# Kernel optimization log

Measured on AMD Instinct MI355X. Metric: run time of the kernel, lower is better.

The kernel has to match this reference:

```python
import jax, jax.numpy as jnp
import numpy as np

N = 100000   # nodes
E = 1600000  # edges (avg degree 16)
IN = 24
HID = 128
OUT = 12


def setup_inputs() -> dict:
    key = jax.random.key(0)
    ks = jax.random.split(key, 16)
    s = 0.05
    return {
        "inputs": jax.random.normal(ks[0], (N, IN), jnp.float32),
        "src": jax.random.randint(ks[1], (E,), 0, N),
        "dst": jax.random.randint(ks[2], (E,), 0, N),
        "e_w": jax.random.uniform(ks[3], (E, 1), jnp.float32),
        "snorm_n": jax.random.uniform(ks[4], (N, 1), jnp.float32),
        "snorm_e": jax.random.uniform(ks[5], (E, 1), jnp.float32),
        "W_emb": jax.random.normal(ks[6], (IN, HID), jnp.float32) * s,
        "b_emb": jnp.zeros((HID,), jnp.float32),
        "W_self1": jax.random.normal(ks[7], (HID, HID), jnp.float32) * s,
        "W1": jax.random.normal(ks[8], (HID, HID), jnp.float32) * s,
        "b1": jnp.zeros((HID,), jnp.float32),
        "W_self2": jax.random.normal(ks[9], (HID, HID), jnp.float32) * s,
        "W2": jax.random.normal(ks[10], (HID, HID), jnp.float32) * s,
        "b2": jnp.zeros((HID,), jnp.float32),
        "W_fc": jax.random.normal(ks[11], (HID, OUT), jnp.float32) * s,
        "b_fc": jnp.zeros((OUT,), jnp.float32),
    }


def _degrees(src, dst):
    out_deg = jnp.clip(jnp.zeros((N,), jnp.float32).at[src].add(1.0), 1.0)
    in_deg = jnp.clip(jnp.zeros((N,), jnp.float32).at[dst].add(1.0), 1.0)
    return out_deg, in_deg


def _gcn_layer(h, src, dst, e_w, out_deg, in_deg, W_self, W, b):
    # self transform (no bias)
    h_s = h @ W_self
    # source-side symmetric norm, edge-weighted message, sum-aggregate at dst
    feat = h * (out_deg ** -0.5)[:, None]          # [N, H]
    m = feat[src] * e_w                            # [E, H]  u_mul_e
    agg = jax.ops.segment_sum(m, dst, num_segments=N)  # [N, H] sum reduce
    h2 = (agg @ W + b) * (in_deg ** -0.5)[:, None]
    return h_s + h2


def reference(inputs, src, dst, e_w, snorm_n, snorm_e,
              W_emb, b_emb, W_self1, W1, b1, W_self2, W2, b2, W_fc, b_fc):
    out_deg, in_deg = _degrees(src, dst)
    h = inputs @ W_emb + b_emb
    h = jax.nn.relu(_gcn_layer(h, src, dst, e_w, out_deg, in_deg, W_self1, W1, b1))
    h = jax.nn.relu(_gcn_layer(h, src, dst, e_w, out_deg, in_deg, W_self2, W2, b2))
    return h @ W_fc + b_fc
```

## Files before the change

### kernel.cpp

```cpp
#include <hip/hip_runtime.h>

#define NN 100000
#define EE 1600000
#define IN_F 24
#define HID 128
#define OUT_F 12
#define LBLK 128

#define NBKT 782
#define PA_BLKS 256
#define PA_EPB 6250

#define OW_BITS 15
#define OWIN 32768
#define OW_GRP 4
#define OW_CPY 64
#define OW_EPB 25000

#define RCAP 2560

#define EMB_B 2048
#define PREP_B 264
#define K1_GRID (PA_BLKS + EMB_B + PREP_B)

typedef unsigned char u8;
typedef unsigned short u16;
typedef unsigned int u32;
typedef unsigned long long u64;

using short8 = __attribute__((ext_vector_type(8))) short;
using f32x4  = __attribute__((ext_vector_type(4))) float;

__device__ __forceinline__ float bf2f(u16 h) {
  return __uint_as_float(((u32)h) << 16);
}
__device__ __forceinline__ u16 f2bf(float f) {
  u32 u = __float_as_uint(f);
  u32 r = (u + 0x7FFFu + ((u >> 16) & 1u)) >> 16;
  return (u16)r;
}
__device__ __forceinline__ float inv_sqrt_cnt(int c) {
  if (c < 1) c = 1;
  return 1.0f / sqrtf((float)c);
}

__global__ __launch_bounds__(256) void k_odeg(const int* __restrict__ src,
                                              u32* __restrict__ whist) {
  __shared__ u32 hist[OWIN / 2];
  int b = blockIdx.x, t = threadIdx.x;
  int g = b >> 6, sb = b & 63;
  for (int i = t; i < OWIN / 2; i += 256) hist[i] = 0;
  __syncthreads();
  int e0 = sb * OW_EPB;
  for (int e = e0 + t; e < e0 + OW_EPB; e += 256) {
    int s = src[e];
    if ((s >> OW_BITS) == g) {
      int i = s & (OWIN - 1);
      atomicAdd(&hist[i >> 1], (i & 1) ? 0x10000u : 1u);
    }
  }
  __syncthreads();
  u32* out = whist + (size_t)b * (OWIN / 2);
  for (int i = t; i < OWIN / 2; i += 256) out[i] = hist[i];
}

__global__ __launch_bounds__(256) void k_onorm(const u32* __restrict__ whist,
                                               float* __restrict__ out_norm) {
  int i = blockIdx.x * 256 + (int)threadIdx.x;
  if (i >= NN / 2) return;
  int n0 = 2 * i;
  int g = n0 >> OW_BITS;
  int pi = (n0 & (OWIN - 1)) >> 1;
  const u32* base = whist + (size_t)(g * OW_CPY) * (OWIN / 2) + pi;
  u32 s = 0;
  #pragma unroll 8
  for (int c = 0; c < OW_CPY; ++c) s += base[(size_t)c * (OWIN / 2)];
  out_norm[n0]     = inv_sqrt_cnt((int)(s & 0xFFFFu));
  out_norm[n0 + 1] = inv_sqrt_cnt((int)(s >> 16));
}

__device__ __forceinline__ void emb_body(int eb, const float* __restrict__ inputs,
                                         const float* __restrict__ W_emb,
                                         const float* __restrict__ b_emb,
                                         u16* __restrict__ harr, float* smemW) {
  int t = threadIdx.x;
  float* Wls = smemW;
  float* bls = smemW + IN_F * HID;
  for (int i = t; i < IN_F * HID; i += 256) Wls[i] = W_emb[i];
  if (t < HID) bls[t] = b_emb[t];
  __syncthreads();
  int c = t & 127;
  int sub = t >> 7;
  for (int node = eb * 2 + sub; node < NN; node += EMB_B * 2) {
    const float* xr = inputs + (size_t)node * IN_F;
    float acc = bls[c];
    #pragma unroll
    for (int k = 0; k < IN_F; ++k) acc = fmaf(xr[k], Wls[k * HID + c], acc);
    harr[(size_t)node * HID + c] = f2bf(acc);
  }
}

__device__ __forceinline__ void prep_body(int pb,
    const float* __restrict__ Ws1, const float* __restrict__ W1m,
    const float* __restrict__ Ws2, const float* __restrict__ W2m,
    const float* __restrict__ Wfc,
    u16* __restrict__ WT1, u16* __restrict__ WT2, u16* __restrict__ WfcT) {
  int idx = pb * 256 + (int)threadIdx.x;
  if (idx < 65536) {
    int layer = idx >> 15;
    int rem = idx & 32767;
    int n = rem >> 8, k = rem & 255;
    const float* A = layer ? Ws2 : Ws1;
    const float* B = layer ? W2m : W1m;
    float v = (k < HID) ? A[(size_t)k * HID + n] : B[(size_t)(k - HID) * HID + n];
    (layer ? WT2 : WT1)[(size_t)n * 256 + k] = f2bf(v);
  } else if (idx < 65536 + 2048) {
    int j = idx - 65536;
    int n = j >> 7, k = j & 127;
    WfcT[(size_t)n * 128 + k] = f2bf(n < OUT_F ? Wfc[(size_t)k * OUT_F + n] : 0.f);
  }
}

__global__ __launch_bounds__(256) void k1(
    const int* __restrict__ dst, u32* __restrict__ histgD,
    const float* __restrict__ inputs, const float* __restrict__ W_emb,
    const float* __restrict__ b_emb, u16* __restrict__ harr,
    const float* __restrict__ Ws1, const float* __restrict__ W1m,
    const float* __restrict__ Ws2, const float* __restrict__ W2m,
    const float* __restrict__ Wfc,
    u16* __restrict__ WT1, u16* __restrict__ WT2, u16* __restrict__ WfcT) {
  __shared__ __align__(16) char sm[13312];
  int b = blockIdx.x, t = threadIdx.x;
  if (b < PA_BLKS) {
    u32* histD = (u32*)sm;
    for (int i = t; i < 1024; i += 256) histD[i] = 0;
    __syncthreads();
    int e0 = b * PA_EPB;
    for (int e = e0 + t; e < e0 + PA_EPB; e += 256)
      atomicAdd(&histD[dst[e] >> 7], 1u);
    __syncthreads();
    for (int i = t; i < 1024; i += 256) histgD[(size_t)b * 1024 + i] = histD[i];
  } else if (b < PA_BLKS + EMB_B) {
    emb_body(b - PA_BLKS, inputs, W_emb, b_emb, harr, (float*)sm);
  } else {
    prep_body(b - PA_BLKS - EMB_B, Ws1, W1m, Ws2, W2m, Wfc, WT1, WT2, WfcT);
  }
}

__global__ __launch_bounds__(256) void k_scan1(u32* __restrict__ histgD,
                                               u32* __restrict__ totalsD) {
  __shared__ u32 s[256];
  int k = blockIdx.x, t = threadIdx.x;
  u32 v = histgD[(size_t)t * 1024 + k];
  s[t] = v;
  __syncthreads();
  for (int off = 1; off < 256; off <<= 1) {
    u32 a = (t >= off) ? s[t - off] : 0;
    __syncthreads();
    s[t] += a;
    __syncthreads();
  }
  histgD[(size_t)t * 1024 + k] = s[t] - v;
  if (t == 255) totalsD[k] = s[255];
}

__global__ __launch_bounds__(1024) void k_scan2(const u32* __restrict__ totalsD,
                                                u32* __restrict__ estartD) {
  __shared__ u32 s[1024];
  int t = threadIdx.x;
  u32 v = (t < NBKT) ? totalsD[t] : 0;
  s[t] = v;
  __syncthreads();
  for (int off = 1; off < 1024; off <<= 1) {
    u32 a = (t >= off) ? s[t - off] : 0;
    __syncthreads();
    s[t] += a;
    __syncthreads();
  }
  if (t < NBKT) estartD[t] = s[t] - v;
  if (t == NBKT - 1) estartD[NBKT] = s[t];
}

__global__ __launch_bounds__(256) void k_passb(
    const int* __restrict__ src, const int* __restrict__ dst,
    const float* __restrict__ e_w,
    const u32* __restrict__ histgD, const u32* __restrict__ estartD,
    u64* __restrict__ ebuf) {
  __shared__ u32 cur[1024];
  int pb = blockIdx.x, t = threadIdx.x;
  for (int i = t; i < 1024; i += 256)
    cur[i] = ((i < NBKT) ? estartD[i] : 0u) + histgD[(size_t)pb * 1024 + i];
  __syncthreads();
  int e0 = pb * PA_EPB;
  for (int e = e0 + t; e < e0 + PA_EPB; e += 256) {
    int s = src[e], d = dst[e];
    u32 hi = (u32)s | (((u32)(d & 127)) << 17);
    u64 rec = ((u64)hi << 32) | (u64)__float_as_uint(e_w[e]);
    u32 pos = atomicAdd(&cur[d >> 7], 1u);
    ebuf[pos] = rec;
  }
}

__global__ __launch_bounds__(256) void k_reorder(
    u64* __restrict__ ebuf, const u32* __restrict__ estart,
    int* __restrict__ row_start, float* __restrict__ in_norm) {
  __shared__ u64 stage[RCAP];
  __shared__ u32 cnt[128], pfx[128], cur[128];
  int k = blockIdx.x, t = threadIdx.x;
  if (t < 128) cnt[t] = 0;
  __syncthreads();
  int e0 = (int)estart[k], e1 = (int)estart[k + 1];
  int n = e1 - e0; if (n > RCAP) n = RCAP;
  for (int i = t; i < n; i += 256) {
    u64 v = ebuf[e0 + i];
    stage[i] = v;
    atomicAdd(&cnt[(u32)(v >> 49) & 127], 1u);
  }
  __syncthreads();
  if (t < 128) pfx[t] = cnt[t];
  __syncthreads();
  for (int off = 1; off < 128; off <<= 1) {
    u32 v = (t < 128 && t >= off) ? pfx[t - off] : 0;
    __syncthreads();
    if (t < 128) pfx[t] += v;
    __syncthreads();
  }
  if (t < 128) {
    u32 start = (u32)e0 + pfx[t] - cnt[t];
    cur[t] = start;
    int node = k * 128 + t;
    if (node < NN) {
      row_start[node] = (int)start;
      in_norm[node] = inv_sqrt_cnt((int)cnt[t]);
    }
  }
  if (k == NBKT - 1 && t == 0) row_start[NN] = e1;
  __syncthreads();
  for (int i = t; i < n; i += 256) {
    u64 v = stage[i];
    u32 pos = atomicAdd(&cur[(u32)(v >> 49) & 127], 1u);
    ebuf[pos] = v;
  }
}

__global__ __launch_bounds__(256) void k_agg(const u16* __restrict__ harr,
                                             const int* __restrict__ row_start,
                                             const float* __restrict__ in_norm,
                                             const float* __restrict__ out_norm,
                                             const u64* __restrict__ ebuf,
                                             u16* __restrict__ aggr) {
  int t = threadIdx.x;
  int node = blockIdx.x * 8 + (t >> 5);
  if (node >= NN) return;
  int lane = t & 31;
  int s0 = row_start[node], s1 = row_start[node + 1];
  float ax = 0.f, ay = 0.f, az = 0.f, aw = 0.f;
  for (int i0 = s0; i0 < s1; i0 += 32) {
    u32 pk2 = 0;
    if (i0 + lane < s1) {
      u64 rec = ebuf[i0 + lane];
      u32 sv = (u32)(rec >> 32) & 0x1FFFF;
      float w = __uint_as_float((u32)rec) * out_norm[sv];
      pk2 = (((u32)f2bf(w)) << 17) | sv;
    }
    int m = s1 - i0; if (m > 32) m = 32;
    int j = 0;
    for (; j + 4 <= m; j += 4) {
      u32 p0 = __shfl(pk2, j,     32);
      u32 p1 = __shfl(pk2, j + 1, 32);
      u32 p2 = __shfl(pk2, j + 2, 32);
      u32 p3 = __shfl(pk2, j + 3, 32);
      ushort4 h0 = *(const ushort4*)(harr + (size_t)(p0 & 0x1FFFF) * HID + lane * 4);
      ushort4 h1 = *(const ushort4*)(harr + (size_t)(p1 & 0x1FFFF) * HID + lane * 4);
      ushort4 h2 = *(const ushort4*)(harr + (size_t)(p2 & 0x1FFFF) * HID + lane * 4);
      ushort4 h3 = *(const ushort4*)(harr + (size_t)(p3 & 0x1FFFF) * HID + lane * 4);
      float w0 = bf2f((u16)(p0 >> 17));
      float w1 = bf2f((u16)(p1 >> 17));
      float w2 = bf2f((u16)(p2 >> 17));
      float w3 = bf2f((u16)(p3 >> 17));
      ax = fmaf(w0, bf2f(h0.x), ax); ay = fmaf(w0, bf2f(h0.y), ay);
      az = fmaf(w0, bf2f(h0.z), az); aw = fmaf(w0, bf2f(h0.w), aw);
      ax = fmaf(w1, bf2f(h1.x), ax); ay = fmaf(w1, bf2f(h1.y), ay);
      az = fmaf(w1, bf2f(h1.z), az); aw = fmaf(w1, bf2f(h1.w), aw);
      ax = fmaf(w2, bf2f(h2.x), ax); ay = fmaf(w2, bf2f(h2.y), ay);
      az = fmaf(w2, bf2f(h2.z), az); aw = fmaf(w2, bf2f(h2.w), aw);
      ax = fmaf(w3, bf2f(h3.x), ax); ay = fmaf(w3, bf2f(h3.y), ay);
      az = fmaf(w3, bf2f(h3.z), az); aw = fmaf(w3, bf2f(h3.w), aw);
    }
    for (; j < m; ++j) {
      u32 p = __shfl(pk2, j, 32);
      float w = bf2f((u16)(p >> 17));
      ushort4 hv = *(const ushort4*)(harr + (size_t)(p & 0x1FFFF) * HID + lane * 4);
      ax = fmaf(w, bf2f(hv.x), ax); ay = fmaf(w, bf2f(hv.y), ay);
      az = fmaf(w, bf2f(hv.z), az); aw = fmaf(w, bf2f(hv.w), aw);
    }
  }
  float inn = in_norm[node];
  ushort4 r;
  r.x = f2bf(ax * inn); r.y = f2bf(ay * inn);
  r.z = f2bf(az * inn); r.w = f2bf(aw * inn);
  *(ushort4*)(aggr + (size_t)node * HID + lane * 4) = r;
}

template<int FC>
__global__ __launch_bounds__(512) void k_layer(u16* __restrict__ harr,
    const u16* __restrict__ aggr,
    const u16* __restrict__ WT, const float* __restrict__ bias,
    const float* __restrict__ in_norm,
    const u16* __restrict__ WfcT, const float* __restrict__ b_fc,
    float* __restrict__ out) {
  __shared__ char smem[135168];
  const int t = threadIdx.x;
  const int r0 = blockIdx.x * LBLK;

  #pragma unroll
  for (int i = 0; i < 4; ++i) {
    int boff = i * 8192 + t * 16;
    int row = boff >> 8, col = boff & 255;
    uint4 v = *(const uint4*)(harr + (size_t)(r0 + row) * HID + (col >> 1));
    *(uint4*)(smem + row * 512 + (col ^ ((row & 7) << 4))) = v;
  }
  #pragma unroll
  for (int i = 0; i < 4; ++i) {
    int boff = i * 8192 + t * 16;
    int row = boff >> 8, col = boff & 255;
    uint4 v = *(const uint4*)(aggr + (size_t)(r0 + row) * HID + (col >> 1));
    *(uint4*)(smem + row * 512 + (256 + (col ^ ((row & 7) << 4)))) = v;
  }
  #pragma unroll
  for (int i = 0; i < 8; ++i) {
    int boff = i * 8192 + t * 16;
    int row = boff >> 9, col = boff & 511;
    uint4 v = *(const uint4*)(WT + (size_t)row * 256 + (col >> 1));
    *(uint4*)(smem + 65536 + row * 512 + (col ^ ((row & 7) << 4))) = v;
  }
  if (FC && t < 256) {
    int row = t >> 4, col = (t & 15) * 16;
    uint4 v = *(const uint4*)(WfcT + (size_t)row * 128 + (col >> 1));
    *(uint4*)(smem + 131072 + row * 256 + (col ^ ((row & 7) << 4))) = v;
  }
  __syncthreads();

  const int lane = t & 63, w = t >> 6;
  const int l15 = lane & 15, lhi = lane >> 4;

  f32x4 acc[8];
  #pragma unroll
  for (int nf = 0; nf < 8; ++nf) acc[nf] = (f32x4){0.f, 0.f, 0.f, 0.f};

  const int arow = w * 16 + l15;
  const char* pa = smem + arow * 512;
  const int aswz = (arow & 7) << 4;
  #pragma unroll
  for (int ks = 0; ks < 8; ++ks) {
    int kb = ks * 64 + (lhi << 4);
    short8 a = *(const short8*)(pa + (kb ^ aswz));
    #pragma unroll
    for (int nf = 0; nf < 8; ++nf) {
      int brow = nf * 16 + l15;
      short8 bf = *(const short8*)(smem + 65536 + brow * 512 + (kb ^ ((brow & 7) << 4)));
      acc[nf] = __builtin_amdgcn_mfma_f32_16x16x32_bf16(a, bf, acc[nf], 0, 0, 0);
    }
  }

  float bcol[8];
  #pragma unroll
  for (int nf = 0; nf < 8; ++nf) bcol[nf] = bias[nf * 16 + l15];

  if (!FC) {
    #pragma unroll
    for (int r = 0; r < 4; ++r) {
      int grow = r0 + w * 16 + (lhi << 2) + r;
      if (grow < NN) {
        float inn = in_norm[grow];
        #pragma unroll
        for (int nf = 0; nf < 8; ++nf) {
          float v = acc[nf][r] + inn * bcol[nf];
          harr[(size_t)grow * HID + nf * 16 + l15] = f2bf(fmaxf(v, 0.f));
        }
      }
    }
  } else {
    __syncthreads();
    #pragma unroll
    for (int r = 0; r < 4; ++r) {
      int lrow = w * 16 + (lhi << 2) + r;
      int grow = r0 + lrow;
      float inn = (grow < NN) ? in_norm[grow] : 0.f;
      #pragma unroll
      for (int nf = 0; nf < 8; ++nf) {
        int col = nf * 16 + l15;
        float v = fmaxf(acc[nf][r] + inn * bcol[nf], 0.f);
        *(u16*)(smem + lrow * 256 + ((col * 2) ^ ((lrow & 7) << 4))) = f2bf(v);
      }
    }
    __syncthreads();
    f32x4 a2 = (f32x4){0.f, 0.f, 0.f, 0.f};
    const char* pa2 = smem + (w * 16 + l15) * 256;
    const int as2 = (l15 & 7) << 4;
    #pragma unroll
    for (int ks = 0; ks < 4; ++ks) {
      int kb = ks * 64 + (lhi << 4);
      short8 a = *(const short8*)(pa2 + (kb ^ as2));
      short8 bf = *(const short8*)(smem + 131072 + l15 * 256 + (kb ^ as2));
      a2 = __builtin_amdgcn_mfma_f32_16x16x32_bf16(a, bf, a2, 0, 0, 0);
    }
    if (l15 < OUT_F) {
      float bo = b_fc[l15];
      #pragma unroll
      for (int r = 0; r < 4; ++r) {
        int grow = r0 + w * 16 + (lhi << 2) + r;
        if (grow < NN) out[(size_t)grow * OUT_F + l15] = a2[r] + bo;
      }
    }
  }
}

extern "C" void kernel_launch(void* const* d_in, const int* in_sizes, int n_in,
                              void* d_out, int out_size, void* d_ws, size_t ws_size,
                              hipStream_t stream) {
  (void)in_sizes; (void)n_in; (void)out_size;
  const float* inputs  = (const float*)d_in[0];
  const int*   src     = (const int*)d_in[1];
  const int*   dst     = (const int*)d_in[2];
  const float* e_w     = (const float*)d_in[3];
  const float* W_emb   = (const float*)d_in[6];
  const float* b_emb   = (const float*)d_in[7];
  const float* W_self1 = (const float*)d_in[8];
  const float* W1      = (const float*)d_in[9];
  const float* b1      = (const float*)d_in[10];
  const float* W_self2 = (const float*)d_in[11];
  const float* W2      = (const float*)d_in[12];
  const float* b2      = (const float*)d_in[13];
  const float* W_fc    = (const float*)d_in[14];
  const float* b_fc    = (const float*)d_in[15];
  float* out = (float*)d_out;

  u32* histgD      = (u32*)d_ws;
  u32* totalsD     = histgD + (size_t)PA_BLKS * 1024;
  u32* estartD     = totalsD + 1024;
  float* out_norm  = (float*)(estartD + 1024);
  float* in_norm   = out_norm + NN;
  int* row_start   = (int*)(in_norm + NN);
  u64* ebuf        = (u64*)(row_start + NN + 4);
  u16* harr        = (u16*)(ebuf + EE);
  u16* aggr        = harr + (size_t)NN * HID;
  u16* WT1         = aggr + (size_t)NN * HID;
  u16* WT2         = WT1 + 32768;
  u16* WfcT        = WT2 + 32768;
  u32* whist       = (u32*)ebuf;

  const size_t NEED = (size_t)PA_BLKS * 1024 * 4 + 2048 * 4 + (size_t)(3 * NN + 4) * 4
                      + (size_t)EE * 8 + (size_t)NN * HID * 4 + (2 * 32768 + 2048) * 2;
  if (ws_size < NEED) return;

  hipLaunchKernelGGL(k_odeg, dim3(OW_GRP * OW_CPY), dim3(256), 0, stream, src, whist);
  hipLaunchKernelGGL(k_onorm, dim3((NN / 2 + 255) / 256), dim3(256), 0, stream,
                     whist, out_norm);
  hipLaunchKernelGGL(k1, dim3(K1_GRID), dim3(256), 0, stream,
                     dst, histgD, inputs, W_emb, b_emb, harr,
                     W_self1, W1, W_self2, W2, W_fc, WT1, WT2, WfcT);
  hipLaunchKernelGGL(k_scan1, dim3(NBKT), dim3(256), 0, stream, histgD, totalsD);
  hipLaunchKernelGGL(k_scan2, dim3(1), dim3(1024), 0, stream, totalsD, estartD);
  hipLaunchKernelGGL(k_passb, dim3(PA_BLKS), dim3(256), 0, stream,
                     src, dst, e_w, histgD, estartD, ebuf);
  hipLaunchKernelGGL(k_reorder, dim3(NBKT), dim3(256), 0, stream,
                     ebuf, estartD, row_start, in_norm);
  hipLaunchKernelGGL(k_agg, dim3((NN + 7) / 8), dim3(256), 0, stream,
                     harr, row_start, in_norm, out_norm, ebuf, aggr);
  hipLaunchKernelGGL(k_layer<0>, dim3((NN + LBLK - 1) / LBLK), dim3(512), 0, stream,
                     harr, aggr, WT1, b1, in_norm, WfcT, b_fc, out);
  hipLaunchKernelGGL(k_agg, dim3((NN + 7) / 8), dim3(256), 0, stream,
                     harr, row_start, in_norm, out_norm, ebuf, aggr);
  hipLaunchKernelGGL(k_layer<1>, dim3((NN + LBLK - 1) / LBLK), dim3(512), 0, stream,
                     harr, aggr, WT2, b2, in_norm, WfcT, b_fc, out);
}
```

Measured before the change: 349.6 us.

## Fuse edge aggregation into the layer GEMM kernel and ping-pong feature buffers

The separate aggregation kernel is removed. Each 128-row layer block now gathers its neighbor sums straight into shared memory before the MFMA GEMM, so the aggregated intermediate never goes to global memory. The out-degree normalization kernel is folded into the k1 multi-role launch, and workspace is reshuffled so layer outputs ping-pong between harr and hb. The cost is that the GEMM blocks must first finish the irregular gather under the occupancy of a 135KB-shared-memory block, which may hurt latency hiding for the gather.

```diff
diff --git a/kernel.cpp b/kernel.cpp
--- a/kernel.cpp
+++ b/kernel.cpp
@@ -17,11 +17,10 @@
 #define OW_CPY 64
 #define OW_EPB 25000
 
-#define RCAP 2560
-
 #define EMB_B 2048
 #define PREP_B 264
-#define K1_GRID (PA_BLKS + EMB_B + PREP_B)
+#define ONORM_B 196
+#define K1_GRID (PA_BLKS + EMB_B + PREP_B + ONORM_B)
 
 typedef unsigned char u8;
 typedef unsigned short u16;
@@ -62,21 +61,6 @@
   __syncthreads();
   u32* out = whist + (size_t)b * (OWIN / 2);
   for (int i = t; i < OWIN / 2; i += 256) out[i] = hist[i];
-}
-
-__global__ __launch_bounds__(256) void k_onorm(const u32* __restrict__ whist,
-                                               float* __restrict__ out_norm) {
-  int i = blockIdx.x * 256 + (int)threadIdx.x;
-  if (i >= NN / 2) return;
-  int n0 = 2 * i;
-  int g = n0 >> OW_BITS;
-  int pi = (n0 & (OWIN - 1)) >> 1;
-  const u32* base = whist + (size_t)(g * OW_CPY) * (OWIN / 2) + pi;
-  u32 s = 0;
-  #pragma unroll 8
-  for (int c = 0; c < OW_CPY; ++c) s += base[(size_t)c * (OWIN / 2)];
-  out_norm[n0]     = inv_sqrt_cnt((int)(s & 0xFFFFu));
-  out_norm[n0 + 1] = inv_sqrt_cnt((int)(s >> 16));
 }
 
 __device__ __forceinline__ void emb_body(int eb, const float* __restrict__ inputs,
@@ -121,6 +105,21 @@
   }
 }
 
+__device__ __forceinline__ void onorm_body(int ob, const u32* __restrict__ whist,
+                                           float* __restrict__ out_norm) {
+  int i = ob * 256 + (int)threadIdx.x;
+  if (i >= NN / 2) return;
+  int n0 = 2 * i;
+  int g = n0 >> OW_BITS;
+  int pi = (n0 & (OWIN - 1)) >> 1;
+  const u32* base = whist + (size_t)(g * OW_CPY) * (OWIN / 2) + pi;
+  u32 s = 0;
+  #pragma unroll 8
+  for (int c = 0; c < OW_CPY; ++c) s += base[(size_t)c * (OWIN / 2)];
+  out_norm[n0]     = inv_sqrt_cnt((int)(s & 0xFFFFu));
+  out_norm[n0 + 1] = inv_sqrt_cnt((int)(s >> 16));
+}
+
 __global__ __launch_bounds__(256) void k1(
     const int* __restrict__ dst, u32* __restrict__ histgD,
     const float* __restrict__ inputs, const float* __restrict__ W_emb,
@@ -128,7 +127,8 @@
     const float* __restrict__ Ws1, const float* __restrict__ W1m,
     const float* __restrict__ Ws2, const float* __restrict__ W2m,
     const float* __restrict__ Wfc,
-    u16* __restrict__ WT1, u16* __restrict__ WT2, u16* __restrict__ WfcT) {
+    u16* __restrict__ WT1, u16* __restrict__ WT2, u16* __restrict__ WfcT,
+    const u32* __restrict__ whist, float* __restrict__ out_norm) {
   __shared__ __align__(16) char sm[13312];
   int b = blockIdx.x, t = threadIdx.x;
   if (b < PA_BLKS) {
@@ -142,8 +142,10 @@
     for (int i = t; i < 1024; i += 256) histgD[(size_t)b * 1024 + i] = histD[i];
   } else if (b < PA_BLKS + EMB_B) {
     emb_body(b - PA_BLKS, inputs, W_emb, b_emb, harr, (float*)sm);
+  } else if (b < PA_BLKS + EMB_B + PREP_B) {
+    prep_body(b - PA_BLKS - EMB_B, Ws1, W1m, Ws2, W2m, Wfc, WT1, WT2, WfcT);
   } else {
-    prep_body(b - PA_BLKS - EMB_B, Ws1, W1m, Ws2, W2m, Wfc, WT1, WT2, WfcT);
+    onorm_body(b - PA_BLKS - EMB_B - PREP_B, whist, out_norm);
   }
 }
 
@@ -201,6 +203,7 @@
   }
 }
 
+#define RCAP 2560
 __global__ __launch_bounds__(256) void k_reorder(
     u64* __restrict__ ebuf, const u32* __restrict__ estart,
     int* __restrict__ row_start, float* __restrict__ in_norm) {
@@ -243,90 +246,18 @@
   }
 }
 
-__global__ __launch_bounds__(256) void k_agg(const u16* __restrict__ harr,
-                                             const int* __restrict__ row_start,
-                                             const float* __restrict__ in_norm,
-                                             const float* __restrict__ out_norm,
-                                             const u64* __restrict__ ebuf,
-                                             u16* __restrict__ aggr) {
-  int t = threadIdx.x;
-  int node = blockIdx.x * 8 + (t >> 5);
-  if (node >= NN) return;
-  int lane = t & 31;
-  int s0 = row_start[node], s1 = row_start[node + 1];
-  float ax = 0.f, ay = 0.f, az = 0.f, aw = 0.f;
-  for (int i0 = s0; i0 < s1; i0 += 32) {
-    u32 pk2 = 0;
-    if (i0 + lane < s1) {
-      u64 rec = ebuf[i0 + lane];
-      u32 sv = (u32)(rec >> 32) & 0x1FFFF;
-      float w = __uint_as_float((u32)rec) * out_norm[sv];
-      pk2 = (((u32)f2bf(w)) << 17) | sv;
-    }
-    int m = s1 - i0; if (m > 32) m = 32;
-    int j = 0;
-    for (; j + 4 <= m; j += 4) {
-      u32 p0 = __shfl(pk2, j,     32);
-      u32 p1 = __shfl(pk2, j + 1, 32);
-      u32 p2 = __shfl(pk2, j + 2, 32);
-      u32 p3 = __shfl(pk2, j + 3, 32);
-      ushort4 h0 = *(const ushort4*)(harr + (size_t)(p0 & 0x1FFFF) * HID + lane * 4);
-      ushort4 h1 = *(const ushort4*)(harr + (size_t)(p1 & 0x1FFFF) * HID + lane * 4);
-      ushort4 h2 = *(const ushort4*)(harr + (size_t)(p2 & 0x1FFFF) * HID + lane * 4);
-      ushort4 h3 = *(const ushort4*)(harr + (size_t)(p3 & 0x1FFFF) * HID + lane * 4);
-      float w0 = bf2f((u16)(p0 >> 17));
-      float w1 = bf2f((u16)(p1 >> 17));
-      float w2 = bf2f((u16)(p2 >> 17));
-      float w3 = bf2f((u16)(p3 >> 17));
-      ax = fmaf(w0, bf2f(h0.x), ax); ay = fmaf(w0, bf2f(h0.y), ay);
-      az = fmaf(w0, bf2f(h0.z), az); aw = fmaf(w0, bf2f(h0.w), aw);
-      ax = fmaf(w1, bf2f(h1.x), ax); ay = fmaf(w1, bf2f(h1.y), ay);
-      az = fmaf(w1, bf2f(h1.z), az); aw = fmaf(w1, bf2f(h1.w), aw);
-      ax = fmaf(w2, bf2f(h2.x), ax); ay = fmaf(w2, bf2f(h2.y), ay);
-      az = fmaf(w2, bf2f(h2.z), az); aw = fmaf(w2, bf2f(h2.w), aw);
-      ax = fmaf(w3, bf2f(h3.x), ax); ay = fmaf(w3, bf2f(h3.y), ay);
-      az = fmaf(w3, bf2f(h3.z), az); aw = fmaf(w3, bf2f(h3.w), aw);
-    }
-    for (; j < m; ++j) {
-      u32 p = __shfl(pk2, j, 32);
-      float w = bf2f((u16)(p >> 17));
-      ushort4 hv = *(const ushort4*)(harr + (size_t)(p & 0x1FFFF) * HID + lane * 4);
-      ax = fmaf(w, bf2f(hv.x), ax); ay = fmaf(w, bf2f(hv.y), ay);
-      az = fmaf(w, bf2f(hv.z), az); aw = fmaf(w, bf2f(hv.w), aw);
-    }
-  }
-  float inn = in_norm[node];
-  ushort4 r;
-  r.x = f2bf(ax * inn); r.y = f2bf(ay * inn);
-  r.z = f2bf(az * inn); r.w = f2bf(aw * inn);
-  *(ushort4*)(aggr + (size_t)node * HID + lane * 4) = r;
-}
-
 template<int FC>
-__global__ __launch_bounds__(512) void k_layer(u16* __restrict__ harr,
-    const u16* __restrict__ aggr,
+__global__ __launch_bounds__(512) void k_fused(const u16* __restrict__ hin,
+    u16* __restrict__ hout,
+    const int* __restrict__ row_start, const float* __restrict__ in_norm,
+    const float* __restrict__ out_norm, const u64* __restrict__ ebuf,
     const u16* __restrict__ WT, const float* __restrict__ bias,
-    const float* __restrict__ in_norm,
     const u16* __restrict__ WfcT, const float* __restrict__ b_fc,
     float* __restrict__ out) {
   __shared__ char smem[135168];
   const int t = threadIdx.x;
   const int r0 = blockIdx.x * LBLK;
 
-  #pragma unroll
-  for (int i = 0; i < 4; ++i) {
-    int boff = i * 8192 + t * 16;
-    int row = boff >> 8, col = boff & 255;
-    uint4 v = *(const uint4*)(harr + (size_t)(r0 + row) * HID + (col >> 1));
-    *(uint4*)(smem + row * 512 + (col ^ ((row & 7) << 4))) = v;
-  }
-  #pragma unroll
-  for (int i = 0; i < 4; ++i) {
-    int boff = i * 8192 + t * 16;
-    int row = boff >> 8, col = boff & 255;
-    uint4 v = *(const uint4*)(aggr + (size_t)(r0 + row) * HID + (col >> 1));
-    *(uint4*)(smem + row * 512 + (256 + (col ^ ((row & 7) << 4)))) = v;
-  }
   #pragma unroll
   for (int i = 0; i < 8; ++i) {
     int boff = i * 8192 + t * 16;
@@ -338,6 +269,68 @@
     int row = t >> 4, col = (t & 15) * 16;
     uint4 v = *(const uint4*)(WfcT + (size_t)row * 128 + (col >> 1));
     *(uint4*)(smem + 131072 + row * 256 + (col ^ ((row & 7) << 4))) = v;
+  }
+  #pragma unroll
+  for (int i = 0; i < 4; ++i) {
+    int boff = i * 8192 + t * 16;
+    int row = boff >> 8, col = boff & 255;
+    uint4 v = *(const uint4*)(hin + (size_t)(r0 + row) * HID + (col >> 1));
+    *(uint4*)(smem + row * 512 + (col ^ ((row & 7) << 4))) = v;
+  }
+
+  {
+    const int grp = t >> 5, lane = t & 31;
+    for (int i = 0; i < 8; ++i) {
+      int lrow = grp * 8 + i;
+      int node = r0 + lrow;
+      float a0 = 0.f, a1 = 0.f, a2 = 0.f, a3 = 0.f;
+      float inn = 0.f;
+      if (node < NN) {
+        inn = in_norm[node];
+        int s0 = row_start[node], s1 = row_start[node + 1];
+        for (int i0 = s0; i0 < s1; i0 += 32) {
+          u32 pk2 = 0;
+          if (i0 + lane < s1) {
+            u64 rec = ebuf[i0 + lane];
+            u32 sv = (u32)(rec >> 32) & 0x1FFFF;
+            float w = __uint_as_float((u32)rec) * out_norm[sv];
+            pk2 = (((u32)f2bf(w)) << 17) | sv;
+          }
+          int m = s1 - i0; if (m > 32) m = 32;
+          int j = 0;
+          for (; j + 8 <= m; j += 8) {
+            ushort4 hv[8]; float wq[8];
+            #pragma unroll
+            for (int q = 0; q < 8; ++q) {
+              u32 p = __shfl(pk2, j + q, 32);
+              wq[q] = bf2f((u16)(p >> 17));
+              hv[q] = *(const ushort4*)(hin + (size_t)(p & 0x1FFFF) * HID + lane * 4);
+            }
+            #pragma unroll
+            for (int q = 0; q < 8; ++q) {
+              a0 = fmaf(wq[q], bf2f(hv[q].x), a0);
+              a1 = fmaf(wq[q], bf2f(hv[q].y), a1);
+              a2 = fmaf(wq[q], bf2f(hv[q].z), a2);
+              a3 = fmaf(wq[q], bf2f(hv[q].w), a3);
+            }
+          }
+          for (; j < m; ++j) {
+            u32 p = __shfl(pk2, j, 32);
+            float w = bf2f((u16)(p >> 17));
+            ushort4 hv = *(const ushort4*)(hin + (size_t)(p & 0x1FFFF) * HID + lane * 4);
+            a0 = fmaf(w, bf2f(hv.x), a0);
+            a1 = fmaf(w, bf2f(hv.y), a1);
+            a2 = fmaf(w, bf2f(hv.z), a2);
+            a3 = fmaf(w, bf2f(hv.w), a3);
+          }
+        }
+      }
+      ushort4 r;
+      r.x = f2bf(a0 * inn); r.y = f2bf(a1 * inn);
+      r.z = f2bf(a2 * inn); r.w = f2bf(a3 * inn);
+      int c2 = lane * 8;
+      *(ushort4*)(smem + lrow * 512 + 256 + (c2 ^ ((lrow & 7) << 4))) = r;
+    }
   }
   __syncthreads();
 
@@ -376,7 +369,7 @@
         #pragma unroll
         for (int nf = 0; nf < 8; ++nf) {
           float v = acc[nf][r] + inn * bcol[nf];
-          harr[(size_t)grow * HID + nf * 16 + l15] = f2bf(fmaxf(v, 0.f));
+          hout[(size_t)grow * HID + nf * 16 + l15] = f2bf(fmaxf(v, 0.f));
         }
       }
     }
@@ -436,42 +429,41 @@
   const float* b_fc    = (const float*)d_in[15];
   float* out = (float*)d_out;
 
-  u32* histgD      = (u32*)d_ws;
-  u32* totalsD     = histgD + (size_t)PA_BLKS * 1024;
-  u32* estartD     = totalsD + 1024;
-  float* out_norm  = (float*)(estartD + 1024);
+  float* out_norm  = (float*)d_ws;
   float* in_norm   = out_norm + NN;
   int* row_start   = (int*)(in_norm + NN);
   u64* ebuf        = (u64*)(row_start + NN + 4);
   u16* harr        = (u16*)(ebuf + EE);
-  u16* aggr        = harr + (size_t)NN * HID;
-  u16* WT1         = aggr + (size_t)NN * HID;
+  u16* WT1         = harr + (size_t)NN * HID;
   u16* WT2         = WT1 + 32768;
   u16* WfcT        = WT2 + 32768;
-  u32* whist       = (u32*)ebuf;
-
-  const size_t NEED = (size_t)PA_BLKS * 1024 * 4 + 2048 * 4 + (size_t)(3 * NN + 4) * 4
-                      + (size_t)EE * 8 + (size_t)NN * HID * 4 + (2 * 32768 + 2048) * 2;
+  char* regZ       = (char*)(WfcT + 2048);
+  u16* hb          = (u16*)regZ;
+  u32* histgD      = (u32*)regZ;
+  u32* totalsD     = histgD + (size_t)PA_BLKS * 1024;
+  u32* estartD     = totalsD + 1024;
+  u32* whist       = estartD + 1024;
+
+  const size_t Z_NEED = (size_t)NN * HID * 2;
+  const size_t NEED = (size_t)(3 * NN + 4) * 4 + (size_t)EE * 8
+                      + (size_t)NN * HID * 2 + (2 * 32768 + 2048) * 2 + Z_NEED;
   if (ws_size < NEED) return;
 
   hipLaunchKernelGGL(k_odeg, dim3(OW_GRP * OW_CPY), dim3(256), 0, stream, src, whist);
-  hipLaunchKernelGGL(k_onorm, dim3((NN / 2 + 255) / 256), dim3(256), 0, stream,
-                     whist, out_norm);
   hipLaunchKernelGGL(k1, dim3(K1_GRID), dim3(256), 0, stream,
                      dst, histgD, inputs, W_emb, b_emb, harr,
-                     W_self1, W1, W_self2, W2, W_fc, WT1, WT2, WfcT);
+                     W_self1, W1, W_self2, W2, W_fc, WT1, WT2, WfcT,
+                     whist, out_norm);
   hipLaunchKernelGGL(k_scan1, dim3(NBKT), dim3(256), 0, stream, histgD, totalsD);
   hipLaunchKernelGGL(k_scan2, dim3(1), dim3(1024), 0, stream, totalsD, estartD);
   hipLaunchKernelGGL(k_passb, dim3(PA_BLKS), dim3(256), 0, stream,
                      src, dst, e_w, histgD, estartD, ebuf);
   hipLaunchKernelGGL(k_reorder, dim3(NBKT), dim3(256), 0, stream,
                      ebuf, estartD, row_start, in_norm);
-  hipLaunchKernelGGL(k_agg, dim3((NN + 7) / 8), dim3(256), 0, stream,
-                     harr, row_start, in_norm, out_norm, ebuf, aggr);
-  hipLaunchKernelGGL(k_layer<0>, dim3((NN + LBLK - 1) / LBLK), dim3(512), 0, stream,
-                     harr, aggr, WT1, b1, in_norm, WfcT, b_fc, out);
-  hipLaunchKernelGGL(k_agg, dim3((NN + 7) / 8), dim3(256), 0, stream,
-                     harr, row_start, in_norm, out_norm, ebuf, aggr);
-  hipLaunchKernelGGL(k_layer<1>, dim3((NN + LBLK - 1) / LBLK), dim3(512), 0, stream,
-                     harr, aggr, WT2, b2, in_norm, WfcT, b_fc, out);
-}
+  hipLaunchKernelGGL(k_fused<0>, dim3(NBKT), dim3(512), 0, stream,
+                     harr, hb, row_start, in_norm, out_norm, ebuf,
+                     WT1, b1, WfcT, b_fc, out);
+  hipLaunchKernelGGL(k_fused<1>, dim3(NBKT), dim3(512), 0, stream,
+                     hb, (u16*)nullptr, row_start, in_norm, out_norm, ebuf,
+                     WT2, b2, WfcT, b_fc, out);
+}
```

New measurement: 441.0 us. 1.26x slower.

## Fold onorm into k1, merge scans via last-block ticket, nontemporal agg I/O

Applied to the files above, without the earlier changes.

Removes two kernel launches. The out-degree norm computation now runs as extra blocks inside k1, and the two scan kernels become one, where the last block to take a ticket computes the bucket prefix. The out-degree histogram uses 32 copies instead of 64, which halves the reduction reads in onorm but doubles the edges each block handles. k_agg now uses nontemporal loads for edge records and a packed nontemporal 64-bit store for aggregates. There is a risk around the ticket location (estartD+1023 overlaps the estartD range, but NBKT is 782, so it is unused) and around the fence ordering for the last-block scan.

```diff
diff --git a/kernel.cpp b/kernel.cpp
--- a/kernel.cpp
+++ b/kernel.cpp
@@ -14,14 +14,15 @@
 #define OW_BITS 15
 #define OWIN 32768
 #define OW_GRP 4
-#define OW_CPY 64
-#define OW_EPB 25000
+#define OW_CPY 32
+#define OW_EPB 50000
 
 #define RCAP 2560
 
 #define EMB_B 2048
 #define PREP_B 264
-#define K1_GRID (PA_BLKS + EMB_B + PREP_B)
+#define ONORM_B 196
+#define K1_GRID (PA_BLKS + EMB_B + PREP_B + ONORM_B)
 
 typedef unsigned char u8;
 typedef unsigned short u16;
@@ -48,7 +49,7 @@
                                               u32* __restrict__ whist) {
   __shared__ u32 hist[OWIN / 2];
   int b = blockIdx.x, t = threadIdx.x;
-  int g = b >> 6, sb = b & 63;
+  int g = b >> 5, sb = b & 31;
   for (int i = t; i < OWIN / 2; i += 256) hist[i] = 0;
   __syncthreads();
   int e0 = sb * OW_EPB;
@@ -62,21 +63,6 @@
   __syncthreads();
   u32* out = whist + (size_t)b * (OWIN / 2);
   for (int i = t; i < OWIN / 2; i += 256) out[i] = hist[i];
-}
-
-__global__ __launch_bounds__(256) void k_onorm(const u32* __restrict__ whist,
-                                               float* __restrict__ out_norm) {
-  int i = blockIdx.x * 256 + (int)threadIdx.x;
-  if (i >= NN / 2) return;
-  int n0 = 2 * i;
-  int g = n0 >> OW_BITS;
-  int pi = (n0 & (OWIN - 1)) >> 1;
-  const u32* base = whist + (size_t)(g * OW_CPY) * (OWIN / 2) + pi;
-  u32 s = 0;
-  #pragma unroll 8
-  for (int c = 0; c < OW_CPY; ++c) s += base[(size_t)c * (OWIN / 2)];
-  out_norm[n0]     = inv_sqrt_cnt((int)(s & 0xFFFFu));
-  out_norm[n0 + 1] = inv_sqrt_cnt((int)(s >> 16));
 }
 
 __device__ __forceinline__ void emb_body(int eb, const float* __restrict__ inputs,
@@ -121,6 +107,21 @@
   }
 }
 
+__device__ __forceinline__ void onorm_body(int ob, const u32* __restrict__ whist,
+                                           float* __restrict__ out_norm) {
+  int i = ob * 256 + (int)threadIdx.x;
+  if (i >= NN / 2) return;
+  int n0 = 2 * i;
+  int g = n0 >> OW_BITS;
+  int pi = (n0 & (OWIN - 1)) >> 1;
+  const u32* base = whist + (size_t)(g * OW_CPY) * (OWIN / 2) + pi;
+  u32 s = 0;
+  #pragma unroll 8
+  for (int c = 0; c < OW_CPY; ++c) s += base[(size_t)c * (OWIN / 2)];
+  out_norm[n0]     = inv_sqrt_cnt((int)(s & 0xFFFFu));
+  out_norm[n0 + 1] = inv_sqrt_cnt((int)(s >> 16));
+}
+
 __global__ __launch_bounds__(256) void k1(
     const int* __restrict__ dst, u32* __restrict__ histgD,
     const float* __restrict__ inputs, const float* __restrict__ W_emb,
@@ -128,9 +129,12 @@
     const float* __restrict__ Ws1, const float* __restrict__ W1m,
     const float* __restrict__ Ws2, const float* __restrict__ W2m,
     const float* __restrict__ Wfc,
-    u16* __restrict__ WT1, u16* __restrict__ WT2, u16* __restrict__ WfcT) {
+    u16* __restrict__ WT1, u16* __restrict__ WT2, u16* __restrict__ WfcT,
+    const u32* __restrict__ whist, float* __restrict__ out_norm,
+    u32* __restrict__ ticket) {
   __shared__ __align__(16) char sm[13312];
   int b = blockIdx.x, t = threadIdx.x;
+  if (b == 0 && t == 0) *ticket = 0;
   if (b < PA_BLKS) {
     u32* histD = (u32*)sm;
     for (int i = t; i < 1024; i += 256) histD[i] = 0;
@@ -142,14 +146,19 @@
     for (int i = t; i < 1024; i += 256) histgD[(size_t)b * 1024 + i] = histD[i];
   } else if (b < PA_BLKS + EMB_B) {
     emb_body(b - PA_BLKS, inputs, W_emb, b_emb, harr, (float*)sm);
+  } else if (b < PA_BLKS + EMB_B + PREP_B) {
+    prep_body(b - PA_BLKS - EMB_B, Ws1, W1m, Ws2, W2m, Wfc, WT1, WT2, WfcT);
   } else {
-    prep_body(b - PA_BLKS - EMB_B, Ws1, W1m, Ws2, W2m, Wfc, WT1, WT2, WfcT);
-  }
-}
-
-__global__ __launch_bounds__(256) void k_scan1(u32* __restrict__ histgD,
-                                               u32* __restrict__ totalsD) {
+    onorm_body(b - PA_BLKS - EMB_B - PREP_B, whist, out_norm);
+  }
+}
+
+__global__ __launch_bounds__(256) void k_scan12(u32* __restrict__ histgD,
+                                                u32* __restrict__ totalsD,
+                                                u32* __restrict__ estartD,
+                                                u32* __restrict__ ticket) {
   __shared__ u32 s[256];
+  __shared__ u32 lastflag;
   int k = blockIdx.x, t = threadIdx.x;
   u32 v = histgD[(size_t)t * 1024 + k];
   s[t] = v;
@@ -162,23 +171,39 @@
   }
   histgD[(size_t)t * 1024 + k] = s[t] - v;
   if (t == 255) totalsD[k] = s[255];
-}
-
-__global__ __launch_bounds__(1024) void k_scan2(const u32* __restrict__ totalsD,
-                                                u32* __restrict__ estartD) {
-  __shared__ u32 s[1024];
-  int t = threadIdx.x;
-  u32 v = (t < NBKT) ? totalsD[t] : 0;
-  s[t] = v;
-  __syncthreads();
-  for (int off = 1; off < 1024; off <<= 1) {
-    u32 a = (t >= off) ? s[t - off] : 0;
-    __syncthreads();
-    s[t] += a;
-    __syncthreads();
-  }
-  if (t < NBKT) estartD[t] = s[t] - v;
-  if (t == NBKT - 1) estartD[NBKT] = s[t];
+  __threadfence();
+  if (t == 0) {
+    u32 old = atomicAdd(ticket, 1u);
+    lastflag = (old == NBKT - 1) ? 1u : 0u;
+  }
+  __syncthreads();
+  if (lastflag) {
+    __threadfence();
+    u32 loc[4];
+    u32 tot = 0;
+    #pragma unroll
+    for (int q = 0; q < 4; ++q) {
+      int idx = t * 4 + q;
+      loc[q] = (idx < NBKT) ? totalsD[idx] : 0;
+      tot += loc[q];
+    }
+    s[t] = tot;
+    __syncthreads();
+    for (int off = 1; off < 256; off <<= 1) {
+      u32 a = (t >= off) ? s[t - off] : 0;
+      __syncthreads();
+      s[t] += a;
+      __syncthreads();
+    }
+    u32 base = s[t] - tot;
+    #pragma unroll
+    for (int q = 0; q < 4; ++q) {
+      int idx = t * 4 + q;
+      if (idx <= NBKT) estartD[idx] = base;
+      base += loc[q];
+    }
+    if (t == 0) *ticket = 0;
+  }
 }
 
 __global__ __launch_bounds__(256) void k_passb(
@@ -258,7 +283,7 @@
   for (int i0 = s0; i0 < s1; i0 += 32) {
     u32 pk2 = 0;
     if (i0 + lane < s1) {
-      u64 rec = ebuf[i0 + lane];
+      u64 rec = __builtin_nontemporal_load(&ebuf[i0 + lane]);
       u32 sv = (u32)(rec >> 32) & 0x1FFFF;
       float w = __uint_as_float((u32)rec) * out_norm[sv];
       pk2 = (((u32)f2bf(w)) << 17) | sv;
@@ -296,10 +321,9 @@
     }
   }
   float inn = in_norm[node];
-  ushort4 r;
-  r.x = f2bf(ax * inn); r.y = f2bf(ay * inn);
-  r.z = f2bf(az * inn); r.w = f2bf(aw * inn);
-  *(ushort4*)(aggr + (size_t)node * HID + lane * 4) = r;
+  u64 pk = (u64)(((u32)f2bf(ay * inn) << 16) | (u32)f2bf(ax * inn))
+         | ((u64)(((u32)f2bf(aw * inn) << 16) | (u32)f2bf(az * inn)) << 32);
+  __builtin_nontemporal_store(pk, (u64*)(aggr + (size_t)node * HID + lane * 4));
 }
 
 template<int FC>
@@ -439,6 +463,7 @@
   u32* histgD      = (u32*)d_ws;
   u32* totalsD     = histgD + (size_t)PA_BLKS * 1024;
   u32* estartD     = totalsD + 1024;
+  u32* ticket      = estartD + 1023;
   float* out_norm  = (float*)(estartD + 1024);
   float* in_norm   = out_norm + NN;
   int* row_start   = (int*)(in_norm + NN);
@@ -455,13 +480,12 @@
   if (ws_size < NEED) return;
 
   hipLaunchKernelGGL(k_odeg, dim3(OW_GRP * OW_CPY), dim3(256), 0, stream, src, whist);
-  hipLaunchKernelGGL(k_onorm, dim3((NN / 2 + 255) / 256), dim3(256), 0, stream,
-                     whist, out_norm);
   hipLaunchKernelGGL(k1, dim3(K1_GRID), dim3(256), 0, stream,
                      dst, histgD, inputs, W_emb, b_emb, harr,
-                     W_self1, W1, W_self2, W2, W_fc, WT1, WT2, WfcT);
-  hipLaunchKernelGGL(k_scan1, dim3(NBKT), dim3(256), 0, stream, histgD, totalsD);
-  hipLaunchKernelGGL(k_scan2, dim3(1), dim3(1024), 0, stream, totalsD, estartD);
+                     W_self1, W1, W_self2, W2, W_fc, WT1, WT2, WfcT,
+                     whist, out_norm, ticket);
+  hipLaunchKernelGGL(k_scan12, dim3(NBKT), dim3(256), 0, stream,
+                     histgD, totalsD, estartD, ticket);
   hipLaunchKernelGGL(k_passb, dim3(PA_BLKS), dim3(256), 0, stream,
                      src, dst, e_w, histgD, estartD, ebuf);
   hipLaunchKernelGGL(k_reorder, dim3(NBKT), dim3(256), 0, stream,
```

Result: slower. 467.9 us (+33.8%).
